# Performance work log

Hardware: AMD Instinct MI355X
Metric: run time of the kernel (lower is better)

The kernel has to match this reference:

```python
import jax, jax.numpy as jnp
import numpy as np

# Dims: batch=2, seqlen=L=384, d_inner=d=384, d_state=s=384, dt_rank=r=384, d_conv=4.
# NOTE: the original torch module only runs when L == d_inner == d_state == dt_rank
# (see its broadcasting in SelectiveScan and the Linear layer plumbing); we reproduce
# that exact (quirky) broadcast faithfully.
B_, L_, D_, S_, R_, K_ = 2, 384, 384, 384, 384, 4


def setup_inputs() -> dict:
    key = jax.random.key(0)
    ks = jax.random.split(key, 9)
    f32 = jnp.float32
    return {
        "x": jax.random.normal(ks[0], (B_, L_, D_), f32),
        "A_log": jax.random.normal(ks[1], (D_, S_), f32) * 0.02,
        "D": jax.random.normal(ks[2], (D_,), f32) * 0.02,
        "dt_w": jax.random.normal(ks[3], (D_, R_), f32) * 0.02,
        "dt_b": jax.random.normal(ks[4], (D_,), f32) * 0.02,
        "B_w": jax.random.normal(ks[5], (S_, D_), f32) * (1.0 / np.sqrt(D_)),
        "C_w": jax.random.normal(ks[6], (S_, D_), f32) * (1.0 / np.sqrt(D_)),
        "conv_w": jax.random.normal(ks[7], (D_, 1, K_), f32) * (1.0 / np.sqrt(K_)),
        "conv_b": jnp.zeros((D_,), f32),
    }


def _forward(x, A_log, D, dt_w, dt_b, B_w, C_w, conv_w, conv_b):
    b, L, d = x.shape
    A = -jnp.exp(A_log)                       # (d, s)
    dt = jax.nn.softplus(x @ dt_w.T + dt_b)   # (b, L, d)
    x_dbl = x @ B_w.T                         # (b, L, s)
    Bm = x_dbl @ B_w.T                        # (b, L, s)  (module applies B_proj twice)
    Cm = x_dbl @ C_w.T                        # (b, L, s)
    # causal depthwise conv1d: pad (k-1) on the left == torch pad k-1 then [:, :, :L]
    xc = jax.lax.conv_general_dilated(
        x.transpose(0, 2, 1), conv_w, (1,), [(conv_w.shape[-1] - 1, 0)],
        feature_group_count=d, dimension_numbers=("NCH", "OIH", "NCH"))
    xc = xc + conv_b[None, :, None]
    u = jax.nn.silu(xc.transpose(0, 2, 1))    # (b, L, d)
    # selective scan (faithful to the torch SelectiveScan broadcasting)
    deltaA = jnp.exp(dt[..., None] * A[None, None])          # (b, L, d, s)
    deltaB_u = dt[..., None] * Bm[:, None, :, :] * u[..., None]  # (b, L, d, s), needs L==d

    def step(h, inp):
        dA_i, dBu_i, C_i, u_i = inp
        h = dA_i * h + dBu_i                  # (b, d, s)
        y = jnp.sum(h * C_i[:, None, :], -1) + u_i * D  # (b, d)
        return h, y

    h0 = jnp.zeros((b, d, deltaA.shape[-1]), x.dtype)
    xs = (deltaA.transpose(1, 0, 2, 3), deltaB_u.transpose(1, 0, 2, 3),
          Cm.transpose(1, 0, 2), u.transpose(1, 0, 2))
    _, ys = jax.lax.scan(step, h0, xs)        # ys: (L, b, d)
    return ys.transpose(1, 0, 2)


def reference(x, A_log, D, dt_w, dt_b, B_w, C_w, conv_w, conv_b):
    return _forward(x, A_log, D, dt_w, dt_b, B_w, C_w, conv_w, conv_b)
```

## Files before the change

kernel.cpp:

```cpp
#include <hip/hip_runtime.h>
#include <math.h>

#define B_SZ 2
#define L_SZ 384
#define D_SZ 384
#define S_SZ 384
#define BLK_ELEMS (L_SZ * D_SZ)
#define TOT_ELEMS (B_SZ * L_SZ * D_SZ)
#define LOG2E 1.4426950408889634f

typedef __attribute__((ext_vector_type(8))) short bf16x8;
typedef __attribute__((ext_vector_type(4))) float f32x4;

__device__ __forceinline__ float fexp2(float x) {
  return __builtin_amdgcn_exp2f(x);
}
__device__ __forceinline__ float softplus_f(float z) {
  return (z > 20.f) ? z : log1pf(__expf(z));
}
__device__ __forceinline__ unsigned short f2bf(float f) {
  unsigned int u = __float_as_uint(f);
  return (unsigned short)((u + 0x7FFFu + ((u >> 16) & 1u)) >> 16);
}
#define PIPELINE_FENCE() asm volatile("" ::: "memory")

__device__ __forceinline__ void g2l16(const void* g, void* l) {
  __builtin_amdgcn_global_load_lds(
      (const __attribute__((address_space(1))) unsigned int*)g,
      (__attribute__((address_space(3))) unsigned int*)l, 16, 0, 0);
}

template <int CTRL>
__device__ __forceinline__ float dpp_mov(float v) {
  return __int_as_float(
      __builtin_amdgcn_update_dpp(0, __float_as_int(v), CTRL, 0xF, 0xF, true));
}

__global__ __launch_bounds__(256) void prep_kernel(
    const float* __restrict__ x, const float* __restrict__ dt_w,
    const float* __restrict__ B_w, const float* __restrict__ C_w,
    const float* __restrict__ cw, const float* __restrict__ cb,
    unsigned short* __restrict__ xbf, unsigned short* __restrict__ dtwbf,
    unsigned short* __restrict__ Bwbf, unsigned short* __restrict__ Cwbf,
    float* __restrict__ u, float* __restrict__ u_t) {
  __shared__ float Tu[32][33];
  const int blk = blockIdx.x;
  if (blk < 720) {
    const float* src;
    unsigned short* dst;
    int base;
    if (blk < 288) { src = x; dst = xbf; base = blk; }
    else if (blk < 432) { src = dt_w; dst = dtwbf; base = blk - 288; }
    else if (blk < 576) { src = B_w; dst = Bwbf; base = blk - 432; }
    else { src = C_w; dst = Cwbf; base = blk - 576; }
    const int idx = base * 1024 + threadIdx.x * 4;
    const float4 v = *(const float4*)(src + idx);
    ushort4 o;
    o.x = f2bf(v.x); o.y = f2bf(v.y); o.z = f2bf(v.z); o.w = f2bf(v.w);
    *(ushort4*)(dst + idx) = o;
    return;
  }
  const int cblk = blk - 720;
  const int b = cblk / 144;
  const int rem = cblk % 144;
  const int iy = rem / 12, lx = rem % 12;
  const int tx = threadIdx.x & 31;
  const int ty = threadIdx.x >> 5;
  const int i0 = iy * 32, l0 = lx * 32;
  const int gi = i0 + tx;
  const float cbv = cb[gi];
  const float cw0 = cw[gi * 4 + 0], cw1 = cw[gi * 4 + 1];
  const float cw2 = cw[gi * 4 + 2], cw3 = cw[gi * 4 + 3];
#pragma unroll
  for (int r = 0; r < 4; ++r) {
    const int l = l0 + ty + 8 * r;
    float acc = cbv;
    const float x3 = x[(b * L_SZ + l) * D_SZ + gi];
    const float x2 = (l >= 1) ? x[(b * L_SZ + l - 1) * D_SZ + gi] : 0.f;
    const float x1 = (l >= 2) ? x[(b * L_SZ + l - 2) * D_SZ + gi] : 0.f;
    const float x0 = (l >= 3) ? x[(b * L_SZ + l - 3) * D_SZ + gi] : 0.f;
    acc = fmaf(x0, cw0, acc);
    acc = fmaf(x1, cw1, acc);
    acc = fmaf(x2, cw2, acc);
    acc = fmaf(x3, cw3, acc);
    const float uv = acc / (1.f + __expf(-acc));
    u[(b * L_SZ + l) * D_SZ + gi] = uv;
    Tu[ty + 8 * r][tx] = uv;
  }
  __syncthreads();
#pragma unroll
  for (int r = 0; r < 4; ++r) {
    const int il = ty + 8 * r;
    u_t[(b * D_SZ + i0 + il) * L_SZ + l0 + tx] = Tu[tx][il];
  }
}

template <int MODE>
__global__ __launch_bounds__(128, 2) void mfma_dual_gemm(
    const unsigned short* __restrict__ Abf,
    const unsigned short* __restrict__ W1bf,
    const unsigned short* __restrict__ W2bf,
    const float* __restrict__ bias,
    float* __restrict__ O1, void* __restrict__ O2v) {
  __shared__ unsigned short sA[32 * 384];
  __shared__ unsigned short sW1[16 * 384];
  __shared__ unsigned short sW2[16 * 384];

  const int t = threadIdx.x;
  const int wv = t >> 6;
  const int lane = t & 63;
  const int nt = blockIdx.x;
  const int mrow = blockIdx.y;

  const unsigned short* Ab = Abf + mrow * 32 * 384;
  const unsigned short* W1b = W1bf + nt * 16 * 384;
  const unsigned short* W2b = W2bf + nt * 16 * 384;

#pragma unroll
  for (int it = 0; it < 12; ++it) {
    const int id = t + it * 128;
    g2l16(Ab + id * 8, (char*)sA + id * 16);
  }
#pragma unroll
  for (int it = 0; it < 6; ++it) {
    const int id = t + it * 128;
    g2l16(W1b + id * 8, (char*)sW1 + id * 16);
    g2l16(W2b + id * 8, (char*)sW2 + id * 16);
  }
  __syncthreads();

  const int rc = lane & 15;
  const int quad = lane >> 4;
  bf16x8 af[12], w1f[12], w2f[12];
#pragma unroll
  for (int kt = 0; kt < 12; ++kt) {
    af[kt] = *(const bf16x8*)&sA[(wv * 16 + rc) * 384 + kt * 32 + quad * 8];
    w1f[kt] = *(const bf16x8*)&sW1[rc * 384 + kt * 32 + quad * 8];
    w2f[kt] = *(const bf16x8*)&sW2[rc * 384 + kt * 32 + quad * 8];
  }
  PIPELINE_FENCE();
  f32x4 acc1 = {0.f, 0.f, 0.f, 0.f};
  f32x4 acc2 = {0.f, 0.f, 0.f, 0.f};
#pragma unroll
  for (int kt = 0; kt < 12; ++kt) {
    acc1 = __builtin_amdgcn_mfma_f32_16x16x32_bf16(af[kt], w1f[kt], acc1, 0, 0, 0);
    acc2 = __builtin_amdgcn_mfma_f32_16x16x32_bf16(af[kt], w2f[kt], acc2, 0, 0, 0);
  }
  const int col = nt * 16 + rc;
  const int row0 = mrow * 32 + wv * 16 + quad * 4;
  if constexpr (MODE == 1) {
    unsigned short* O2 = (unsigned short*)O2v;
    const float bb = bias[col];
    const int b = row0 / L_SZ;
    const int lb = row0 - b * L_SZ;
#pragma unroll
    for (int r = 0; r < 4; ++r) {
      O1[(b * D_SZ + col) * L_SZ + lb + r] = softplus_f(acc1[r] + bb);
      O2[(row0 + r) * 384 + col] = f2bf(acc2[r]);
    }
  } else {
    float* O2 = (float*)O2v;
#pragma unroll
    for (int r = 0; r < 4; ++r) {
      O1[(row0 + r) * 384 + col] = acc1[r];
      O2[(row0 + r) * 384 + col] = acc2[r];
    }
  }
}

struct ChunkS {
  f32x4 d0, d1, u0, u1;
  float c[8];
};

#define LOAD_CHUNK(K, B0, B1, B2, DTB, DUB)                                    \
  {                                                                            \
    asm volatile("global_load_dwordx4 %0, %1, off" : "=v"(K.d0) : "v"(DTB));   \
    asm volatile("global_load_dwordx4 %0, %1, off offset:16"                   \
                 : "=v"(K.d1) : "v"(DTB));                                     \
    asm volatile("global_load_dwordx4 %0, %1, off" : "=v"(K.u0) : "v"(DUB));   \
    asm volatile("global_load_dwordx4 %0, %1, off offset:16"                   \
                 : "=v"(K.u1) : "v"(DUB));                                     \
    asm volatile("global_load_dword %0, %1, off" : "=v"(K.c[0]) : "v"(B0));    \
    asm volatile("global_load_dword %0, %1, off offset:1536"                   \
                 : "=v"(K.c[1]) : "v"(B0));                                    \
    asm volatile("global_load_dword %0, %1, off offset:3072"                   \
                 : "=v"(K.c[2]) : "v"(B0));                                    \
    asm volatile("global_load_dword %0, %1, off" : "=v"(K.c[3]) : "v"(B1));    \
    asm volatile("global_load_dword %0, %1, off offset:1536"                   \
                 : "=v"(K.c[4]) : "v"(B1));                                    \
    asm volatile("global_load_dword %0, %1, off offset:3072"                   \
                 : "=v"(K.c[5]) : "v"(B1));                                    \
    asm volatile("global_load_dword %0, %1, off" : "=v"(K.c[6]) : "v"(B2));    \
    asm volatile("global_load_dword %0, %1, off offset:1536"                   \
                 : "=v"(K.c[7]) : "v"(B2));                                    \
  }

#define WAIT_CHUNK(K)                                                          \
  asm volatile("s_waitcnt vmcnt(24)"                                           \
               : "+v"(K.d0), "+v"(K.d1), "+v"(K.u0), "+v"(K.u1),               \
                 "+v"(K.c[0]), "+v"(K.c[1]), "+v"(K.c[2]), "+v"(K.c[3]),       \
                 "+v"(K.c[4]), "+v"(K.c[5]), "+v"(K.c[6]), "+v"(K.c[7]))

#define ADV_BASES()                                                            \
  { cb0 += 3072; cb1 += 3072; cb2 += 3072; dtB += 8; duB += 8; }

__global__ __launch_bounds__(64, 4) void scan_kernel(
    const float* __restrict__ A_log, const float* __restrict__ dt_t,
    const float* __restrict__ u_t, const float* __restrict__ Bm,
    const float* __restrict__ Cm, float* __restrict__ part) {
  const int wave = blockIdx.x;
  const int lane = threadIdx.x;
  const int w = wave % 6;
  const int sid = wave / 6;
  const int b = sid / D_SZ;
  const int i = sid % D_SZ;
  const int j = w * 64 + lane;

  const float a2 = -__expf(A_log[i * S_SZ + j]) * LOG2E;
  const float bw = Bm[(b * D_SZ + i) * S_SZ + j];
  float h = 0.f;

  const float* dtB = dt_t + (b * D_SZ + i) * L_SZ;
  const float* duB = u_t + (b * D_SZ + i) * L_SZ;
  const float* cmrow = Cm + b * BLK_ELEMS + j;
  const float* cb0 = cmrow;
  const float* cb1 = cmrow + 3 * D_SZ;
  const float* cb2 = cmrow + 6 * D_SZ;

  const int sq = (((lane >> 3) & 1) << 2) | (((lane >> 2) & 1) << 1) | (lane & 1);
  const bool storer = (lane & 0x32) == 0;
  float* pstore = part + ((w * B_SZ + b) * D_SZ + i) * L_SZ + sq;

  asm volatile("" :: "v"(a2), "v"(bw));
  asm volatile("s_waitcnt vmcnt(0)");

  auto compute_chunk = [&](ChunkS& K) {
    float acc[8];
    const float dts[8] = {K.d0[0], K.d0[1], K.d0[2], K.d0[3],
                          K.d1[0], K.d1[1], K.d1[2], K.d1[3]};
    const float us[8] = {K.u0[0], K.u0[1], K.u0[2], K.u0[3],
                         K.u1[0], K.u1[1], K.u1[2], K.u1[3]};
#pragma unroll
    for (int s = 0; s < 8; ++s) {
      const float e = fexp2(dts[s] * a2);
      h = fmaf(e, h, bw * (dts[s] * us[s]));
      acc[s] = h * K.c[s];
    }
    {
      const bool hi = (lane & 8) != 0;
#pragma unroll
      for (int q = 0; q < 4; ++q) {
        const float keep = hi ? acc[q + 4] : acc[q];
        const float send = hi ? acc[q] : acc[q + 4];
        acc[q] = keep + dpp_mov<0x140>(send);
      }
    }
    {
      const bool hi = (lane & 4) != 0;
#pragma unroll
      for (int q = 0; q < 2; ++q) {
        const float keep = hi ? acc[q + 2] : acc[q];
        const float send = hi ? acc[q] : acc[q + 2];
        acc[q] = keep + dpp_mov<0x141>(send);
      }
    }
    {
      const bool hi = (lane & 1) != 0;
      const float keep = hi ? acc[1] : acc[0];
      const float send = hi ? acc[0] : acc[1];
      acc[0] = keep + dpp_mov<0xB1>(send);
    }
    float r = acc[0];
    r += __shfl_xor(r, 2, 64);
    r += __shfl_xor(r, 16, 64);
    r += __shfl_xor(r, 32, 64);
    if (storer) *pstore = r;
    pstore += 8;
  };

  ChunkS K0, K1, K2;
  LOAD_CHUNK(K0, cb0, cb1, cb2, dtB, duB);
  ADV_BASES();
  LOAD_CHUNK(K1, cb0, cb1, cb2, dtB, duB);
  ADV_BASES();
#pragma unroll 1
  for (int it = 0; it < 16; ++it) {
    LOAD_CHUNK(K2, cb0, cb1, cb2, dtB, duB);
    ADV_BASES();
    WAIT_CHUNK(K0);
    compute_chunk(K0);
    LOAD_CHUNK(K0, cb0, cb1, cb2, dtB, duB);
    ADV_BASES();
    WAIT_CHUNK(K1);
    compute_chunk(K1);
    LOAD_CHUNK(K1, cb0, cb1, cb2, dtB, duB);
    ADV_BASES();
    WAIT_CHUNK(K2);
    compute_chunk(K2);
  }
}

__global__ __launch_bounds__(256) void combine_kernel(
    const float* __restrict__ part, const float* __restrict__ u,
    const float* __restrict__ Dv, float* __restrict__ y) {
  __shared__ float T[32][33];
  const int tx = threadIdx.x;
  const int ty0 = threadIdx.y;
  const int b = blockIdx.z;
  const int i0 = blockIdx.y * 32;
  const int l0 = blockIdx.x * 32;
#pragma unroll
  for (int r = 0; r < 4; ++r) {
    const int il = ty0 + 8 * r;
    float s = 0.f;
#pragma unroll
    for (int w = 0; w < 6; ++w)
      s += part[((w * B_SZ + b) * D_SZ + i0 + il) * L_SZ + l0 + tx];
    T[il][tx] = s;
  }
  __syncthreads();
#pragma unroll
  for (int r = 0; r < 4; ++r) {
    const int ll = ty0 + 8 * r;
    const int gi = i0 + tx;
    const int off = (b * L_SZ + l0 + ll) * D_SZ + gi;
    y[off] = fmaf(u[off], Dv[gi], T[tx][ll]);
  }
}

extern "C" void kernel_launch(void* const* d_in, const int* in_sizes, int n_in,
                              void* d_out, int out_size, void* d_ws,
                              size_t ws_size, hipStream_t stream) {
  const float* x = (const float*)d_in[0];
  const float* A_log = (const float*)d_in[1];
  const float* D = (const float*)d_in[2];
  const float* dt_w = (const float*)d_in[3];
  const float* dt_b = (const float*)d_in[4];
  const float* B_w = (const float*)d_in[5];
  const float* C_w = (const float*)d_in[6];
  const float* conv_w = (const float*)d_in[7];
  const float* conv_b = (const float*)d_in[8];
  float* y = (float*)d_out;

  float* ws = (float*)d_ws;
  float* u = ws;
  float* Bm = ws + TOT_ELEMS;
  float* Cm = ws + 2 * TOT_ELEMS;
  float* dt_t = ws + 3 * TOT_ELEMS;
  float* u_t = ws + 4 * TOT_ELEMS;
  float* part = ws + 5 * TOT_ELEMS;
  unsigned short* bfarea = (unsigned short*)(ws + 11 * TOT_ELEMS);
  unsigned short* xbf = bfarea;
  unsigned short* dtwbf = bfarea + 294912;
  unsigned short* Bwbf = bfarea + 442368;
  unsigned short* Cwbf = bfarea + 589824;
  unsigned short* xdblbf = bfarea + 737280;

  prep_kernel<<<1008, 256, 0, stream>>>(x, dt_w, B_w, C_w, conv_w, conv_b,
                                        xbf, dtwbf, Bwbf, Cwbf, u, u_t);
  mfma_dual_gemm<1><<<dim3(24, 24), 128, 0, stream>>>(xbf, dtwbf, Bwbf, dt_b,
                                                      dt_t, xdblbf);
  mfma_dual_gemm<2><<<dim3(24, 24), 128, 0, stream>>>(xdblbf, Bwbf, Cwbf,
                                                      nullptr, Bm, Cm);
  scan_kernel<<<6 * B_SZ * D_SZ, 64, 0, stream>>>(A_log, dt_t, u_t, Bm, Cm, part);
  combine_kernel<<<dim3(L_SZ / 32, D_SZ / 32, B_SZ), dim3(32, 8), 0, stream>>>(
      part, u, D, y);
}
```

Baseline: 139.7 us.

## Remove combine kernel via atomic accumulation into output, precompute dt*u in GEMM

```diff
diff --git a/kernel.cpp b/kernel.cpp
--- a/kernel.cpp
+++ b/kernel.cpp
@@ -40,10 +40,10 @@
     const float* __restrict__ x, const float* __restrict__ dt_w,
     const float* __restrict__ B_w, const float* __restrict__ C_w,
     const float* __restrict__ cw, const float* __restrict__ cb,
+    const float* __restrict__ Dv,
     unsigned short* __restrict__ xbf, unsigned short* __restrict__ dtwbf,
     unsigned short* __restrict__ Bwbf, unsigned short* __restrict__ Cwbf,
-    float* __restrict__ u, float* __restrict__ u_t) {
-  __shared__ float Tu[32][33];
+    float* __restrict__ u, float* __restrict__ y) {
   const int blk = blockIdx.x;
   if (blk < 720) {
     const float* src;
@@ -66,9 +66,10 @@
   const int iy = rem / 12, lx = rem % 12;
   const int tx = threadIdx.x & 31;
   const int ty = threadIdx.x >> 5;
-  const int i0 = iy * 32, l0 = lx * 32;
-  const int gi = i0 + tx;
+  const int gi = iy * 32 + tx;
+  const int l0 = lx * 32;
   const float cbv = cb[gi];
+  const float Di = Dv[gi];
   const float cw0 = cw[gi * 4 + 0], cw1 = cw[gi * 4 + 1];
   const float cw2 = cw[gi * 4 + 2], cw3 = cw[gi * 4 + 3];
 #pragma unroll
@@ -84,14 +85,9 @@
     acc = fmaf(x2, cw2, acc);
     acc = fmaf(x3, cw3, acc);
     const float uv = acc / (1.f + __expf(-acc));
-    u[(b * L_SZ + l) * D_SZ + gi] = uv;
-    Tu[ty + 8 * r][tx] = uv;
-  }
-  __syncthreads();
-#pragma unroll
-  for (int r = 0; r < 4; ++r) {
-    const int il = ty + 8 * r;
-    u_t[(b * D_SZ + i0 + il) * L_SZ + l0 + tx] = Tu[tx][il];
+    const int off = (b * L_SZ + l) * D_SZ + gi;
+    u[off] = uv;
+    y[off] = uv * Di;
   }
 }
 
@@ -100,8 +96,9 @@
     const unsigned short* __restrict__ Abf,
     const unsigned short* __restrict__ W1bf,
     const unsigned short* __restrict__ W2bf,
-    const float* __restrict__ bias,
-    float* __restrict__ O1, void* __restrict__ O2v) {
+    const float* __restrict__ bias, const float* __restrict__ u,
+    float* __restrict__ O1, float* __restrict__ O1b,
+    void* __restrict__ O2v) {
   __shared__ unsigned short sA[32 * 384];
   __shared__ unsigned short sW1[16 * 384];
   __shared__ unsigned short sW2[16 * 384];
@@ -153,9 +150,13 @@
     const float bb = bias[col];
     const int b = row0 / L_SZ;
     const int lb = row0 - b * L_SZ;
+    const int tro = (b * D_SZ + col) * L_SZ + lb;
 #pragma unroll
     for (int r = 0; r < 4; ++r) {
-      O1[(b * D_SZ + col) * L_SZ + lb + r] = softplus_f(acc1[r] + bb);
+      const float dtv = softplus_f(acc1[r] + bb);
+      const float uu = u[(row0 + r) * 384 + col];
+      O1[tro + r] = dtv;
+      O1b[tro + r] = dtv * uu;
       O2[(row0 + r) * 384 + col] = f2bf(acc2[r]);
     }
   } else {
@@ -207,8 +208,8 @@
 
 __global__ __launch_bounds__(64, 4) void scan_kernel(
     const float* __restrict__ A_log, const float* __restrict__ dt_t,
-    const float* __restrict__ u_t, const float* __restrict__ Bm,
-    const float* __restrict__ Cm, float* __restrict__ part) {
+    const float* __restrict__ dtu_t, const float* __restrict__ Bm,
+    const float* __restrict__ Cm, float* __restrict__ y) {
   const int wave = blockIdx.x;
   const int lane = threadIdx.x;
   const int w = wave % 6;
@@ -222,7 +223,7 @@
   float h = 0.f;
 
   const float* dtB = dt_t + (b * D_SZ + i) * L_SZ;
-  const float* duB = u_t + (b * D_SZ + i) * L_SZ;
+  const float* duB = dtu_t + (b * D_SZ + i) * L_SZ;
   const float* cmrow = Cm + b * BLK_ELEMS + j;
   const float* cb0 = cmrow;
   const float* cb1 = cmrow + 3 * D_SZ;
@@ -230,7 +231,7 @@
 
   const int sq = (((lane >> 3) & 1) << 2) | (((lane >> 2) & 1) << 1) | (lane & 1);
   const bool storer = (lane & 0x32) == 0;
-  float* pstore = part + ((w * B_SZ + b) * D_SZ + i) * L_SZ + sq;
+  float* pstore = y + b * BLK_ELEMS + sq * D_SZ + i;
 
   asm volatile("" :: "v"(a2), "v"(bw));
   asm volatile("s_waitcnt vmcnt(0)");
@@ -239,12 +240,12 @@
     float acc[8];
     const float dts[8] = {K.d0[0], K.d0[1], K.d0[2], K.d0[3],
                           K.d1[0], K.d1[1], K.d1[2], K.d1[3]};
-    const float us[8] = {K.u0[0], K.u0[1], K.u0[2], K.u0[3],
-                         K.u1[0], K.u1[1], K.u1[2], K.u1[3]};
+    const float dus[8] = {K.u0[0], K.u0[1], K.u0[2], K.u0[3],
+                          K.u1[0], K.u1[1], K.u1[2], K.u1[3]};
 #pragma unroll
     for (int s = 0; s < 8; ++s) {
       const float e = fexp2(dts[s] * a2);
-      h = fmaf(e, h, bw * (dts[s] * us[s]));
+      h = fmaf(e, h, bw * dus[s]);
       acc[s] = h * K.c[s];
     }
     {
@@ -272,11 +273,11 @@
       acc[0] = keep + dpp_mov<0xB1>(send);
     }
     float r = acc[0];
-    r += __shfl_xor(r, 2, 64);
+    r += dpp_mov<0x4E>(r);
     r += __shfl_xor(r, 16, 64);
     r += __shfl_xor(r, 32, 64);
-    if (storer) *pstore = r;
-    pstore += 8;
+    if (storer) atomicAdd(pstore, r);
+    pstore += 8 * D_SZ;
   };
 
   ChunkS K0, K1, K2;
@@ -301,34 +302,6 @@
   }
 }
 
-__global__ __launch_bounds__(256) void combine_kernel(
-    const float* __restrict__ part, const float* __restrict__ u,
-    const float* __restrict__ Dv, float* __restrict__ y) {
-  __shared__ float T[32][33];
-  const int tx = threadIdx.x;
-  const int ty0 = threadIdx.y;
-  const int b = blockIdx.z;
-  const int i0 = blockIdx.y * 32;
-  const int l0 = blockIdx.x * 32;
-#pragma unroll
-  for (int r = 0; r < 4; ++r) {
-    const int il = ty0 + 8 * r;
-    float s = 0.f;
-#pragma unroll
-    for (int w = 0; w < 6; ++w)
-      s += part[((w * B_SZ + b) * D_SZ + i0 + il) * L_SZ + l0 + tx];
-    T[il][tx] = s;
-  }
-  __syncthreads();
-#pragma unroll
-  for (int r = 0; r < 4; ++r) {
-    const int ll = ty0 + 8 * r;
-    const int gi = i0 + tx;
-    const int off = (b * L_SZ + l0 + ll) * D_SZ + gi;
-    y[off] = fmaf(u[off], Dv[gi], T[tx][ll]);
-  }
-}
-
 extern "C" void kernel_launch(void* const* d_in, const int* in_sizes, int n_in,
                               void* d_out, int out_size, void* d_ws,
                               size_t ws_size, hipStream_t stream) {
@@ -348,22 +321,19 @@
   float* Bm = ws + TOT_ELEMS;
   float* Cm = ws + 2 * TOT_ELEMS;
   float* dt_t = ws + 3 * TOT_ELEMS;
-  float* u_t = ws + 4 * TOT_ELEMS;
-  float* part = ws + 5 * TOT_ELEMS;
-  unsigned short* bfarea = (unsigned short*)(ws + 11 * TOT_ELEMS);
+  float* dtu_t = ws + 4 * TOT_ELEMS;
+  unsigned short* bfarea = (unsigned short*)(ws + 5 * TOT_ELEMS);
   unsigned short* xbf = bfarea;
   unsigned short* dtwbf = bfarea + 294912;
   unsigned short* Bwbf = bfarea + 442368;
   unsigned short* Cwbf = bfarea + 589824;
   unsigned short* xdblbf = bfarea + 737280;
 
-  prep_kernel<<<1008, 256, 0, stream>>>(x, dt_w, B_w, C_w, conv_w, conv_b,
-                                        xbf, dtwbf, Bwbf, Cwbf, u, u_t);
-  mfma_dual_gemm<1><<<dim3(24, 24), 128, 0, stream>>>(xbf, dtwbf, Bwbf, dt_b,
-                                                      dt_t, xdblbf);
-  mfma_dual_gemm<2><<<dim3(24, 24), 128, 0, stream>>>(xdblbf, Bwbf, Cwbf,
-                                                      nullptr, Bm, Cm);
-  scan_kernel<<<6 * B_SZ * D_SZ, 64, 0, stream>>>(A_log, dt_t, u_t, Bm, Cm, part);
-  combine_kernel<<<dim3(L_SZ / 32, D_SZ / 32, B_SZ), dim3(32, 8), 0, stream>>>(
-      part, u, D, y);
-}
+  prep_kernel<<<1008, 256, 0, stream>>>(x, dt_w, B_w, C_w, conv_w, conv_b, D,
+                                        xbf, dtwbf, Bwbf, Cwbf, u, y);
+  mfma_dual_gemm<1><<<dim3(24, 24), 128, 0, stream>>>(
+      xbf, dtwbf, Bwbf, dt_b, u, dt_t, dtu_t, xdblbf);
+  mfma_dual_gemm<2><<<dim3(24, 24), 128, 0, stream>>>(
+      xdblbf, Bwbf, Cwbf, nullptr, nullptr, Bm, nullptr, Cm);
+  scan_kernel<<<6 * B_SZ * D_SZ, 64, 0, stream>>>(A_log, dt_t, dtu_t, Bm, Cm, y);
+}
```

Result: slower. 217.4 us (+55.7%).
